# Kernel tuning notes

Hardware: AMD Instinct MI355X
Metric: run time of the kernel (lower is better)

Reference implementation:

```python
import jax, jax.numpy as jnp
import numpy as np

B, T, D_MODEL, HEAD_DIM = 8, 2048, 1024, 128


def setup_inputs() -> dict:
    key = jax.random.key(0)
    k1, k2, k3, k4 = jax.random.split(key, 4)
    scale = 1.0 / np.sqrt(D_MODEL)
    return {
        "x": jax.random.normal(k1, (B, T, D_MODEL), dtype=jnp.float32),
        "Wq": jax.random.normal(k2, (HEAD_DIM, D_MODEL), dtype=jnp.float32) * scale,
        "Wk": jax.random.normal(k3, (HEAD_DIM, D_MODEL), dtype=jnp.float32) * scale,
        "Wv": jax.random.normal(k4, (HEAD_DIM, D_MODEL), dtype=jnp.float32) * scale,
    }


def reference(x, Wq, Wk, Wv) -> jnp.ndarray:
    # x: [B, T, C]; torch Linear(no bias): y = x @ W.T, W: [head_dim, d_model]
    q = jnp.einsum("btc,hc->bth", x, Wq)  # [B, T, H]
    k = jnp.einsum("btc,hc->bth", x, Wk)
    v = jnp.einsum("btc,hc->bth", x, Wv)
    head_dim = Wq.shape[0]
    scores = jnp.einsum("bqh,bkh->bqk", q, k) / jnp.sqrt(jnp.float32(head_dim))  # [B, T, T]
    T_ = x.shape[1]
    causal = jnp.tril(jnp.ones((T_, T_), dtype=bool))
    scores = jnp.where(causal, scores, -jnp.inf)
    probs = jax.nn.softmax(scores, axis=-1)
    # dropout is identity at inference (eval mode)
    out = jnp.einsum("bqk,bkh->bqh", probs, v)  # [B, T, head_dim]
    return out
```

## Files before the change

kernel.cpp:

```cpp
#include <hip/hip_runtime.h>
#include <hip/hip_bf16.h>
#include <math.h>

#define T_ 2048
#define C_ 1024
#define H_ 128
#define NB 8
#define WN 131072
#define SC 0.08838834764831845f

typedef __attribute__((ext_vector_type(8))) short bf16x8;
typedef __attribute__((ext_vector_type(8))) unsigned short u16x8;
typedef __attribute__((ext_vector_type(4))) float f32x4;

#define MFMA16(a,b,c) __builtin_amdgcn_mfma_f32_16x16x32_bf16((a),(b),(c),0,0,0)

__device__ __forceinline__ unsigned short f2bf(float f) {
    union { float f; unsigned u; } v; v.f = f;
    unsigned r = v.u + 0x7fffu + ((v.u >> 16) & 1u);
    return (unsigned short)(r >> 16);
}
__device__ __forceinline__ float bf2f(unsigned short u) {
    union { unsigned u; float f; } v; v.u = ((unsigned)u) << 16; return v.f;
}
__device__ __forceinline__ unsigned pk2bf(float a, float b) {
    __hip_bfloat162 h = __float22bfloat162_rn(float2{a, b});
    union { __hip_bfloat162 h; unsigned u; } v; v.h = h; return v.u;
}
__device__ __forceinline__ void gld16(void* lds, const void* g) {
    __builtin_amdgcn_global_load_lds(
        (const __attribute__((address_space(1))) unsigned*)g,
        (__attribute__((address_space(3))) unsigned*)lds, 16, 0, 0);
}

__global__ __launch_bounds__(256) void wconv(const float* __restrict__ Wq,
                                             const float* __restrict__ Wk,
                                             const float* __restrict__ Wv,
                                             unsigned short* __restrict__ Wb) {
    int e = (blockIdx.x * 256 + threadIdx.x) * 8;
    int which = e >> 17;
    int off = e & (WN - 1);
    const float* src = (which == 0) ? Wq : (which == 1 ? Wk : Wv);
    float s = (which == 0) ? SC : 1.0f;
    const float4* p = (const float4*)(src + off);
    float4 a = p[0], b = p[1];
    uint4 o = { pk2bf(a.x * s, a.y * s), pk2bf(a.z * s, a.w * s),
                pk2bf(b.x * s, b.y * s), pk2bf(b.z * s, b.w * s) };
    *(uint4*)(Wb + e) = o;
}

__global__ __launch_bounds__(256, 2) void proj(const float* __restrict__ x,
                                               const unsigned short* __restrict__ Wb,
                                               unsigned short* __restrict__ Q,
                                               unsigned short* __restrict__ K,
                                               unsigned short* __restrict__ V) {
    __shared__ unsigned short Xs[2][64][64];
    __shared__ unsigned short Ws[2][192][64];

    const int tid  = threadIdx.x;
    const int wave = tid >> 6, lane = tid & 63;
    const int quad = lane >> 4, l16 = lane & 15;
    const int wm   = wave >> 1, wn = wave & 1;
    const int m0   = (blockIdx.x >> 1) * 64;
    const int n0   = (blockIdx.x & 1) * 192;

    f32x4 acc[2][6];
    #pragma unroll
    for (int i = 0; i < 2; i++)
        #pragma unroll
        for (int j = 0; j < 6; j++) acc[i][j] = {0.f, 0.f, 0.f, 0.f};

    const int xrow = tid >> 2, xcg = tid & 3;
    const float* xg = x + (size_t)(m0 + xrow) * C_ + xcg * 16;
    const int xk = xrow & 7;
    const int key = l16 & 7;
    const unsigned short* wg = Wb + (size_t)(n0 + wave * 48 + (lane >> 3)) * C_
                               + (size_t)(((lane & 7) ^ (lane >> 3)) * 8);

    float4 xA[4], xB[4];

    #define WISSUE(buf, kc) do {                                                  \
        _Pragma("unroll")                                                         \
        for (int i = 0; i < 6; i++)                                               \
            gld16(&Ws[buf][wave * 48 + i * 8][0], wg + (size_t)i * 8 * C_ + (kc));\
    } while (0)

    #define XLOAD(dst, kc) do {                                                   \
        const float* xp = xg + (kc);                                              \
        dst[0] = *(const float4*)xp;        dst[1] = *(const float4*)(xp + 4);    \
        dst[2] = *(const float4*)(xp + 8);  dst[3] = *(const float4*)(xp + 12);   \
    } while (0)

    #define XWR(buf, src) do {                                                    \
        uint4 u0 = { pk2bf(src[0].x, src[0].y), pk2bf(src[0].z, src[0].w),        \
                     pk2bf(src[1].x, src[1].y), pk2bf(src[1].z, src[1].w) };      \
        uint4 u1 = { pk2bf(src[2].x, src[2].y), pk2bf(src[2].z, src[2].w),        \
                     pk2bf(src[3].x, src[3].y), pk2bf(src[3].z, src[3].w) };      \
        *(uint4*)&Xs[buf][xrow][((2 * xcg)     ^ xk) * 8] = u0;                   \
        *(uint4*)&Xs[buf][xrow][((2 * xcg + 1) ^ xk) * 8] = u1;                   \
    } while (0)

    #define COMPUTE(buf) do {                                                     \
        bf16x8 af[2][2];                                                          \
        _Pragma("unroll")                                                         \
        for (int kk = 0; kk < 2; kk++)                                            \
            _Pragma("unroll")                                                     \
            for (int mf = 0; mf < 2; mf++)                                        \
                af[mf][kk] = *(bf16x8*)&Xs[buf][wm * 32 + mf * 16 + l16]          \
                                          [((kk * 4 + quad) ^ key) * 8];          \
        _Pragma("unroll")                                                         \
        for (int kk = 0; kk < 2; kk++)                                            \
            _Pragma("unroll")                                                     \
            for (int nf = 0; nf < 6; nf++) {                                      \
                bf16x8 bq = *(bf16x8*)&Ws[buf][wn * 96 + nf * 16 + l16]           \
                                         [((kk * 4 + quad) ^ key) * 8];           \
                acc[0][nf] = MFMA16(af[0][kk], bq, acc[0][nf]);                   \
                acc[1][nf] = MFMA16(af[1][kk], bq, acc[1][nf]);                   \
            }                                                                     \
    } while (0)

    #define BAR4 do {                                                             \
        asm volatile("s_waitcnt vmcnt(4) lgkmcnt(0)" ::: "memory");               \
        __builtin_amdgcn_s_barrier();                                             \
        __builtin_amdgcn_sched_barrier(0);                                        \
    } while (0)
    #define BAR0 do {                                                             \
        asm volatile("s_waitcnt vmcnt(0) lgkmcnt(0)" ::: "memory");               \
        __builtin_amdgcn_s_barrier();                                             \
        __builtin_amdgcn_sched_barrier(0);                                        \
    } while (0)
    #define PIN __builtin_amdgcn_sched_barrier(0)

    XLOAD(xA, 0);
    WISSUE(0, 0);
    PIN;
    XLOAD(xB, 64);
    XWR(0, xA);

    for (int t = 0; t < 7; t++) {
        BAR4;
        WISSUE(1, (2 * t + 1) * 64);
        PIN;
        XLOAD(xA, (2 * t + 2) * 64);
        COMPUTE(0);
        XWR(1, xB);
        BAR4;
        WISSUE(0, (2 * t + 2) * 64);
        PIN;
        XLOAD(xB, (2 * t + 3) * 64);
        COMPUTE(1);
        XWR(0, xA);
    }
    BAR4;
    WISSUE(1, 15 * 64);
    COMPUTE(0);
    XWR(1, xB);
    BAR0;
    COMPUTE(1);

    #undef WISSUE
    #undef XLOAD
    #undef XWR
    #undef COMPUTE
    #undef BAR4
    #undef BAR0
    #undef PIN

    #pragma unroll
    for (int nf = 0; nf < 6; nf++) {
        int nb = n0 + wn * 96 + nf * 16;
        int which = nb >> 7;
        unsigned short* dst = (which == 0) ? Q : (which == 1 ? K : V);
        int c = (nb & 127) + l16;
        #pragma unroll
        for (int mf = 0; mf < 2; mf++)
            #pragma unroll
            for (int r = 0; r < 4; r++)
                dst[(size_t)(m0 + wm * 32 + mf * 16 + quad * 4 + r) * H_ + c] = f2bf(acc[mf][nf][r]);
    }
}

__global__ __launch_bounds__(256, 3) void attn(const unsigned short* __restrict__ Qg,
                                               const unsigned short* __restrict__ Kg,
                                               const unsigned short* __restrict__ Vg,
                                               unsigned short* __restrict__ Ob,
                                               float* __restrict__ Ml) {
    const int bid = blockIdx.x;
    const int b   = bid & 7;
    const int j   = bid >> 3;
    int g = 0;
    while (j >= 2 * (g + 1) * (g + 2)) g++;
    const int within = j - 2 * g * (g + 1);
    const int t = within / (g + 1);
    const int s = within - t * (g + 1);
    const int qt = 4 * g + t;
    const int qbase = qt * 64, kstart = s * 256;
    const int kend  = (kstart + 256 < qbase + 64) ? kstart + 256 : qbase + 64;
    const int niter = (kend - kstart) >> 6;

    __shared__ unsigned short Ks[4][64][32];
    __shared__ unsigned short Vt[128 * 64];
    __shared__ unsigned short Ps[4][16][64];

    const int tid = threadIdx.x, wave = tid >> 6, lane = tid & 63;
    const int quad = lane >> 4, l16 = lane & 15;
    const size_t base = (size_t)b * T_ * H_;

    const unsigned short* ksrc = Kg + base + (size_t)(kstart + (lane >> 2)) * H_ + wave * 32 + (lane & 3) * 8;
    #pragma unroll
    for (int p = 0; p < 4; p++) gld16(&Ks[wave][p * 16][0], ksrc + (size_t)p * 16 * H_);
    const unsigned short* vsrc = Vg + base + (size_t)(kstart + wave * 8 + quad * 2) * H_ + l16 * 8;
    u16x8 vr[2][2];
    vr[0][0] = *(const u16x8*)vsrc;             vr[0][1] = *(const u16x8*)(vsrc + H_);
    vr[1][0] = *(const u16x8*)(vsrc + 32 * H_); vr[1][1] = *(const u16x8*)(vsrc + 33 * H_);

    bf16x8 qf[4];
    const unsigned short* qp = Qg + base + (size_t)(qbase + wave * 16 + l16) * H_ + quad * 8;
    #pragma unroll
    for (int kk = 0; kk < 4; kk++) qf[kk] = *(const bf16x8*)(qp + kk * 32);

    f32x4 o[8];
    #pragma unroll
    for (int i = 0; i < 8; i++) o[i] = {0.f, 0.f, 0.f, 0.f};
    float m_i = -INFINITY, l_i = 0.f;
    const int swz = (l16 & 7) << 3;
    const int qg = qbase + wave * 16 + l16;

    __syncthreads();

    #pragma unroll
    for (int g2 = 0; g2 < 2; g2++) {
        int t0 = wave * 8 + g2 * 32 + quad * 2;
        int t8 = t0 >> 3;
        #pragma unroll
        for (int jj = 0; jj < 8; jj++) {
            int h = l16 * 8 + jj;
            unsigned pk = (unsigned)(unsigned short)vr[g2][0][jj] | ((unsigned)(unsigned short)vr[g2][1][jj] << 16);
            int blk = (t8 ^ (h & 7) ^ ((h >> 3) & 7)) & 7;
            *(unsigned*)&Vt[h * 64 + blk * 8 + (t0 & 7)] = pk;
        }
    }

    for (int kt = 0; ; kt++) {
        const int kbase = kstart + kt * 64;
        f32x4 st[4];
        #pragma unroll
        for (int nf = 0; nf < 4; nf++) st[nf] = {0.f, 0.f, 0.f, 0.f};
        #pragma unroll
        for (int kk = 0; kk < 4; kk++)
            #pragma unroll
            for (int nf = 0; nf < 4; nf++) {
                bf16x8 kfr = *(bf16x8*)&Ks[kk][nf * 16 + l16][quad * 8];
                st[nf] = MFMA16(kfr, qf[kk], st[nf]);
            }
        if (kbase + 64 > qbase) {
            #pragma unroll
            for (int nf = 0; nf < 4; nf++) {
                int kg = kbase + nf * 16 + quad * 4;
                #pragma unroll
                for (int r = 0; r < 4; r++)
                    if (kg + r > qg) st[nf][r] = -INFINITY;
            }
        }
        float mx = st[0][0];
        #pragma unroll
        for (int nf = 0; nf < 4; nf++)
            #pragma unroll
            for (int r = 0; r < 4; r++) mx = fmaxf(mx, st[nf][r]);
        mx = fmaxf(mx, __shfl_xor(mx, 16, 64));
        mx = fmaxf(mx, __shfl_xor(mx, 32, 64));
        float mnew = fmaxf(m_i, mx);
        float al = __expf(m_i - mnew);
        m_i = mnew;
        float rs = 0.f;
        #pragma unroll
        for (int nf = 0; nf < 4; nf++)
            #pragma unroll
            for (int r = 0; r < 4; r++) {
                float e = __expf(st[nf][r] - mnew);
                st[nf][r] = e; rs += e;
            }
        rs += __shfl_xor(rs, 16, 64);
        rs += __shfl_xor(rs, 32, 64);
        l_i = al * l_i + rs;
        #pragma unroll
        for (int nf = 0; nf < 4; nf++) {
            uint2 pk = { pk2bf(st[nf][0], st[nf][1]), pk2bf(st[nf][2], st[nf][3]) };
            *(uint2*)&Ps[wave][l16][(nf * 16 + quad * 4) ^ swz] = pk;
        }
        float a0 = __shfl(al, quad * 4 + 0, 64), a1 = __shfl(al, quad * 4 + 1, 64);
        float a2 = __shfl(al, quad * 4 + 2, 64), a3 = __shfl(al, quad * 4 + 3, 64);
        #pragma unroll
        for (int i = 0; i < 8; i++) {
            o[i][0] *= a0; o[i][1] *= a1; o[i][2] *= a2; o[i][3] *= a3;
        }
        __syncthreads();

        const bool more = (kt + 1 < niter);
        if (more) {
            ksrc += 64 * H_;
            #pragma unroll
            for (int p = 0; p < 4; p++) gld16(&Ks[wave][p * 16][0], ksrc + (size_t)p * 16 * H_);
            vsrc += 64 * H_;
            vr[0][0] = *(const u16x8*)vsrc;             vr[0][1] = *(const u16x8*)(vsrc + H_);
            vr[1][0] = *(const u16x8*)(vsrc + 32 * H_); vr[1][1] = *(const u16x8*)(vsrc + 33 * H_);
        }
        bf16x8 pa0 = *(bf16x8*)&Ps[wave][l16][(quad * 8) ^ swz];
        bf16x8 pa1 = *(bf16x8*)&Ps[wave][l16][(32 + quad * 8) ^ swz];
        #pragma unroll
        for (int nf = 0; nf < 8; nf++) {
            int h = nf * 16 + l16;
            int ex = (h & 7) ^ ((h >> 3) & 7);
            bf16x8 v0 = *(bf16x8*)&Vt[h * 64 + ((quad ^ ex) & 7) * 8];
            bf16x8 v1 = *(bf16x8*)&Vt[h * 64 + (((quad + 4) ^ ex) & 7) * 8];
            o[nf] = MFMA16(pa0, v0, o[nf]);
            o[nf] = MFMA16(pa1, v1, o[nf]);
        }
        if (!more) break;
        __syncthreads();
        #pragma unroll
        for (int g2 = 0; g2 < 2; g2++) {
            int t0 = wave * 8 + g2 * 32 + quad * 2;
            int t8 = t0 >> 3;
            #pragma unroll
            for (int jj = 0; jj < 8; jj++) {
                int h = l16 * 8 + jj;
                unsigned pk = (unsigned)(unsigned short)vr[g2][0][jj] | ((unsigned)(unsigned short)vr[g2][1][jj] << 16);
                int blk = (t8 ^ (h & 7) ^ ((h >> 3) & 7)) & 7;
                *(unsigned*)&Vt[h * 64 + blk * 8 + (t0 & 7)] = pk;
            }
        }
    }

    const int slot = j * NB + b;
    float lq[4];
    #pragma unroll
    for (int r = 0; r < 4; r++) lq[r] = __shfl(l_i, quad * 4 + r, 64);
    const size_t obase = (size_t)slot * 64 * 128;
    #pragma unroll
    for (int r = 0; r < 4; r++) {
        float invl = 1.0f / lq[r];
        #pragma unroll
        for (int nf = 0; nf < 8; nf++)
            Ob[obase + (size_t)(wave * 16 + quad * 4 + r) * 128 + nf * 16 + l16] = f2bf(o[nf][r] * invl);
    }
    if (lane < 16) {
        int ridx = slot * 64 + wave * 16 + l16;
        Ml[ridx * 2]     = m_i;
        Ml[ridx * 2 + 1] = l_i;
    }
}

__global__ __launch_bounds__(256) void merge(const unsigned short* __restrict__ Ob,
                                             const float* __restrict__ Ml,
                                             float* __restrict__ out) {
    const int qt = blockIdx.x, b = blockIdx.y;
    const int g = qt >> 2;
    const int Pq = 2 * g * (g + 1) + (qt & 3) * (g + 1);
    const int ns = g + 1;
    const int tid = threadIdx.x;
    const int row = tid >> 2, c0 = (tid & 3) * 32;

    float mv[8], lv[8], mg = -INFINITY;
    for (int s2 = 0; s2 < ns; s2++) {
        int slot = (Pq + s2) * NB + b;
        mv[s2] = Ml[(slot * 64 + row) * 2];
        lv[s2] = Ml[(slot * 64 + row) * 2 + 1];
        mg = fmaxf(mg, mv[s2]);
    }
    float L = 0.f, w[8];
    for (int s2 = 0; s2 < ns; s2++) { w[s2] = lv[s2] * __expf(mv[s2] - mg); L += w[s2]; }
    float inv = 1.0f / L;

    float accv[32];
    #pragma unroll
    for (int i = 0; i < 32; i++) accv[i] = 0.f;
    for (int s2 = 0; s2 < ns; s2++) {
        int slot = (Pq + s2) * NB + b;
        const unsigned short* op = Ob + ((size_t)(slot * 64 + row)) * 128 + c0;
        #pragma unroll
        for (int cc = 0; cc < 4; cc++) {
            u16x8 v = *(const u16x8*)(op + cc * 8);
            #pragma unroll
            for (int jj = 0; jj < 8; jj++) accv[cc * 8 + jj] += w[s2] * bf2f(v[jj]);
        }
    }
    float* od = out + ((size_t)(b * T_ + qt * 64 + row)) * 128 + c0;
    #pragma unroll
    for (int cc = 0; cc < 8; cc++) {
        float4 w4 = { accv[cc*4] * inv, accv[cc*4+1] * inv, accv[cc*4+2] * inv, accv[cc*4+3] * inv };
        *(float4*)(od + cc * 4) = w4;
    }
}

extern "C" void kernel_launch(void* const* d_in, const int* in_sizes, int n_in,
                              void* d_out, int out_size, void* d_ws, size_t ws_size,
                              hipStream_t stream) {
    const float* x  = (const float*)d_in[0];
    const float* Wq = (const float*)d_in[1];
    const float* Wk = (const float*)d_in[2];
    const float* Wv = (const float*)d_in[3];

    char* ws = (char*)d_ws;
    unsigned short* Wb = (unsigned short*)ws;
    unsigned short* Q  = (unsigned short*)(ws + (size_t) 1 * (1u << 20));
    unsigned short* K  = (unsigned short*)(ws + (size_t) 5 * (1u << 20));
    unsigned short* V  = (unsigned short*)(ws + (size_t) 9 * (1u << 20));
    unsigned short* Ob = (unsigned short*)(ws + (size_t)13 * (1u << 20));
    float*          Ml = (float*)(ws + (size_t)32 * (1u << 20));
    float* out = (float*)d_out;

    hipLaunchKernelGGL(wconv, dim3(192), dim3(256), 0, stream, Wq, Wk, Wv, Wb);
    hipLaunchKernelGGL(proj,  dim3(512), dim3(256), 0, stream, x, Wb, Q, K, V);
    hipLaunchKernelGGL(attn,  dim3(1152), dim3(256), 0, stream, Q, K, V, Ob, Ml);
    hipLaunchKernelGGL(merge, dim3(32, NB), dim3(256), 0, stream, Ob, Ml, out);
}
```

Before: 159.4 us.

## Widen attention blocks to 128 query rows with 512-key splits; remap proj blocks

```diff
diff --git a/kernel.cpp b/kernel.cpp
--- a/kernel.cpp
+++ b/kernel.cpp
@@ -61,8 +61,9 @@
     const int wave = tid >> 6, lane = tid & 63;
     const int quad = lane >> 4, l16 = lane & 15;
     const int wm   = wave >> 1, wn = wave & 1;
-    const int m0   = (blockIdx.x >> 1) * 64;
-    const int n0   = (blockIdx.x & 1) * 192;
+    const int bid  = blockIdx.x;
+    const int m0   = (((bid >> 4) << 3) | (bid & 7)) * 64;
+    const int n0   = ((bid >> 3) & 1) * 192;
 
     f32x4 acc[2][6];
     #pragma unroll
@@ -180,7 +181,7 @@
     }
 }
 
-__global__ __launch_bounds__(256, 3) void attn(const unsigned short* __restrict__ Qg,
+__global__ __launch_bounds__(512, 6) void attn(const unsigned short* __restrict__ Qg,
                                                const unsigned short* __restrict__ Kg,
                                                const unsigned short* __restrict__ Vg,
                                                unsigned short* __restrict__ Ob,
@@ -194,25 +195,26 @@
     const int t = within / (g + 1);
     const int s = within - t * (g + 1);
     const int qt = 4 * g + t;
-    const int qbase = qt * 64, kstart = s * 256;
-    const int kend  = (kstart + 256 < qbase + 64) ? kstart + 256 : qbase + 64;
+    const int qbase = qt * 128, kstart = s * 512;
+    const int kend  = (kstart + 512 < qbase + 128) ? kstart + 512 : qbase + 128;
     const int niter = (kend - kstart) >> 6;
 
     __shared__ unsigned short Ks[4][64][32];
     __shared__ unsigned short Vt[128 * 64];
-    __shared__ unsigned short Ps[4][16][64];
+    __shared__ unsigned short Ps[8][16][64];
 
     const int tid = threadIdx.x, wave = tid >> 6, lane = tid & 63;
     const int quad = lane >> 4, l16 = lane & 15;
     const size_t base = (size_t)b * T_ * H_;
 
-    const unsigned short* ksrc = Kg + base + (size_t)(kstart + (lane >> 2)) * H_ + wave * 32 + (lane & 3) * 8;
-    #pragma unroll
-    for (int p = 0; p < 4; p++) gld16(&Ks[wave][p * 16][0], ksrc + (size_t)p * 16 * H_);
+    const int kch = wave & 3, krh = wave >> 2;
+    const unsigned short* ksrc = Kg + base + (size_t)(kstart + krh * 32 + (lane >> 2)) * H_
+                               + kch * 32 + (lane & 3) * 8;
+    #pragma unroll
+    for (int p = 0; p < 2; p++) gld16(&Ks[kch][krh * 32 + p * 16][0], ksrc + (size_t)p * 16 * H_);
     const unsigned short* vsrc = Vg + base + (size_t)(kstart + wave * 8 + quad * 2) * H_ + l16 * 8;
-    u16x8 vr[2][2];
-    vr[0][0] = *(const u16x8*)vsrc;             vr[0][1] = *(const u16x8*)(vsrc + H_);
-    vr[1][0] = *(const u16x8*)(vsrc + 32 * H_); vr[1][1] = *(const u16x8*)(vsrc + 33 * H_);
+    u16x8 vr[2];
+    vr[0] = *(const u16x8*)vsrc; vr[1] = *(const u16x8*)(vsrc + H_);
 
     bf16x8 qf[4];
     const unsigned short* qp = Qg + base + (size_t)(qbase + wave * 16 + l16) * H_ + quad * 8;
@@ -225,21 +227,21 @@
     float m_i = -INFINITY, l_i = 0.f;
     const int swz = (l16 & 7) << 3;
     const int qg = qbase + wave * 16 + l16;
-
+    const int qw = qbase + wave * 16;
+
+    #define VTWRITE() do {                                                           \
+        _Pragma("unroll")                                                            \
+        for (int jj = 0; jj < 8; jj++) {                                             \
+            int h = l16 * 8 + jj;                                                    \
+            unsigned pk = (unsigned)(unsigned short)vr[0][jj]                        \
+                        | ((unsigned)(unsigned short)vr[1][jj] << 16);               \
+            int blk = (wave ^ (h & 7) ^ ((h >> 3) & 7)) & 7;                         \
+            *(unsigned*)&Vt[h * 64 + blk * 8 + quad * 2] = pk;                       \
+        }                                                                            \
+    } while (0)
+
+    VTWRITE();
     __syncthreads();
-
-    #pragma unroll
-    for (int g2 = 0; g2 < 2; g2++) {
-        int t0 = wave * 8 + g2 * 32 + quad * 2;
-        int t8 = t0 >> 3;
-        #pragma unroll
-        for (int jj = 0; jj < 8; jj++) {
-            int h = l16 * 8 + jj;
-            unsigned pk = (unsigned)(unsigned short)vr[g2][0][jj] | ((unsigned)(unsigned short)vr[g2][1][jj] << 16);
-            int blk = (t8 ^ (h & 7) ^ ((h >> 3) & 7)) & 7;
-            *(unsigned*)&Vt[h * 64 + blk * 8 + (t0 & 7)] = pk;
-        }
-    }
 
     for (int kt = 0; ; kt++) {
         const int kbase = kstart + kt * 64;
@@ -253,7 +255,7 @@
                 bf16x8 kfr = *(bf16x8*)&Ks[kk][nf * 16 + l16][quad * 8];
                 st[nf] = MFMA16(kfr, qf[kk], st[nf]);
             }
-        if (kbase + 64 > qbase) {
+        if (kbase + 64 > qw) {
             #pragma unroll
             for (int nf = 0; nf < 4; nf++) {
                 int kg = kbase + nf * 16 + quad * 4;
@@ -300,10 +302,9 @@
         if (more) {
             ksrc += 64 * H_;
             #pragma unroll
-            for (int p = 0; p < 4; p++) gld16(&Ks[wave][p * 16][0], ksrc + (size_t)p * 16 * H_);
+            for (int p = 0; p < 2; p++) gld16(&Ks[kch][krh * 32 + p * 16][0], ksrc + (size_t)p * 16 * H_);
             vsrc += 64 * H_;
-            vr[0][0] = *(const u16x8*)vsrc;             vr[0][1] = *(const u16x8*)(vsrc + H_);
-            vr[1][0] = *(const u16x8*)(vsrc + 32 * H_); vr[1][1] = *(const u16x8*)(vsrc + 33 * H_);
+            vr[0] = *(const u16x8*)vsrc; vr[1] = *(const u16x8*)(vsrc + H_);
         }
         bf16x8 pa0 = *(bf16x8*)&Ps[wave][l16][(quad * 8) ^ swz];
         bf16x8 pa1 = *(bf16x8*)&Ps[wave][l16][(32 + quad * 8) ^ swz];
@@ -318,25 +319,15 @@
         }
         if (!more) break;
         __syncthreads();
-        #pragma unroll
-        for (int g2 = 0; g2 < 2; g2++) {
-            int t0 = wave * 8 + g2 * 32 + quad * 2;
-            int t8 = t0 >> 3;
-            #pragma unroll
-            for (int jj = 0; jj < 8; jj++) {
-                int h = l16 * 8 + jj;
-                unsigned pk = (unsigned)(unsigned short)vr[g2][0][jj] | ((unsigned)(unsigned short)vr[g2][1][jj] << 16);
-                int blk = (t8 ^ (h & 7) ^ ((h >> 3) & 7)) & 7;
-                *(unsigned*)&Vt[h * 64 + blk * 8 + (t0 & 7)] = pk;
-            }
-        }
-    }
+        VTWRITE();
+    }
+    #undef VTWRITE
 
     const int slot = j * NB + b;
     float lq[4];
     #pragma unroll
     for (int r = 0; r < 4; r++) lq[r] = __shfl(l_i, quad * 4 + r, 64);
-    const size_t obase = (size_t)slot * 64 * 128;
+    const size_t obase = (size_t)slot * 128 * 128;
     #pragma unroll
     for (int r = 0; r < 4; r++) {
         float invl = 1.0f / lq[r];
@@ -345,7 +336,7 @@
             Ob[obase + (size_t)(wave * 16 + quad * 4 + r) * 128 + nf * 16 + l16] = f2bf(o[nf][r] * invl);
     }
     if (lane < 16) {
-        int ridx = slot * 64 + wave * 16 + l16;
+        int ridx = slot * 128 + wave * 16 + l16;
         Ml[ridx * 2]     = m_i;
         Ml[ridx * 2 + 1] = l_i;
     }
@@ -354,21 +345,22 @@
 __global__ __launch_bounds__(256) void merge(const unsigned short* __restrict__ Ob,
                                              const float* __restrict__ Ml,
                                              float* __restrict__ out) {
-    const int qt = blockIdx.x, b = blockIdx.y;
+    const int bx = blockIdx.x, b = blockIdx.y;
+    const int qt = bx >> 1, rh = bx & 1;
     const int g = qt >> 2;
     const int Pq = 2 * g * (g + 1) + (qt & 3) * (g + 1);
     const int ns = g + 1;
     const int tid = threadIdx.x;
-    const int row = tid >> 2, c0 = (tid & 3) * 32;
-
-    float mv[8], lv[8], mg = -INFINITY;
+    const int row = rh * 64 + (tid >> 2), c0 = (tid & 3) * 32;
+
+    float mv[4], lv[4], mg = -INFINITY;
     for (int s2 = 0; s2 < ns; s2++) {
         int slot = (Pq + s2) * NB + b;
-        mv[s2] = Ml[(slot * 64 + row) * 2];
-        lv[s2] = Ml[(slot * 64 + row) * 2 + 1];
+        mv[s2] = Ml[(slot * 128 + row) * 2];
+        lv[s2] = Ml[(slot * 128 + row) * 2 + 1];
         mg = fmaxf(mg, mv[s2]);
     }
-    float L = 0.f, w[8];
+    float L = 0.f, w[4];
     for (int s2 = 0; s2 < ns; s2++) { w[s2] = lv[s2] * __expf(mv[s2] - mg); L += w[s2]; }
     float inv = 1.0f / L;
 
@@ -377,7 +369,7 @@
     for (int i = 0; i < 32; i++) accv[i] = 0.f;
     for (int s2 = 0; s2 < ns; s2++) {
         int slot = (Pq + s2) * NB + b;
-        const unsigned short* op = Ob + ((size_t)(slot * 64 + row)) * 128 + c0;
+        const unsigned short* op = Ob + ((size_t)(slot * 128 + row)) * 128 + c0;
         #pragma unroll
         for (int cc = 0; cc < 4; cc++) {
             u16x8 v = *(const u16x8*)(op + cc * 8);
@@ -385,7 +377,7 @@
             for (int jj = 0; jj < 8; jj++) accv[cc * 8 + jj] += w[s2] * bf2f(v[jj]);
         }
     }
-    float* od = out + ((size_t)(b * T_ + qt * 64 + row)) * 128 + c0;
+    float* od = out + ((size_t)(b * T_ + qt * 128 + row)) * 128 + c0;
     #pragma unroll
     for (int cc = 0; cc < 8; cc++) {
         float4 w4 = { accv[cc*4] * inv, accv[cc*4+1] * inv, accv[cc*4+2] * inv, accv[cc*4+3] * inv };
@@ -412,6 +404,6 @@
 
     hipLaunchKernelGGL(wconv, dim3(192), dim3(256), 0, stream, Wq, Wk, Wv, Wb);
     hipLaunchKernelGGL(proj,  dim3(512), dim3(256), 0, stream, x, Wb, Q, K, V);
-    hipLaunchKernelGGL(attn,  dim3(1152), dim3(256), 0, stream, Q, K, V, Ob, Ml);
+    hipLaunchKernelGGL(attn,  dim3(320), dim3(512), 0, stream, Q, K, V, Ob, Ml);
     hipLaunchKernelGGL(merge, dim3(32, NB), dim3(256), 0, stream, Ob, Ml, out);
 }
```

Result: slower. 262.1 us (+64.4%).
